# Optimization experiments

Hardware: AMD Instinct MI355X
Metric: run time of the kernel (lower is better)

The kernel has to match this reference:

```python
import jax, jax.numpy as jnp
import numpy as np


def _patch_desc(x, patch_size):
    # x: (n, c, h, w). Replicate-pad by patch_size//2 and gather all
    # patch_size*patch_size shifted views -> (n, c*p*p, h*w) descriptors.
    n, c, h, w = x.shape
    step = patch_size // 2
    y = jnp.pad(x, ((0, 0), (0, 0), (step, step), (step, step)), mode='edge')
    feats = [y[:, :, i:i + h, j:j + w]
             for i in range(patch_size) for j in range(patch_size)]
    d = jnp.stack(feats, axis=2)            # (n, c, p*p, h, w)
    return d.reshape(n, c * patch_size * patch_size, h * w)


def setup_inputs() -> dict:
    key = jax.random.key(0)
    k1, k2 = jax.random.split(key)
    n, c, h, w = 4, 16, 64, 64
    s = jax.random.normal(k1, (n, c, h, w), dtype=jnp.float32)
    t = jax.random.normal(k2, (n, c, h, w), dtype=jnp.float32)
    return {"s": s, "t": t, "patch_size": 3}


def reference(s, t, patch_size):
    n, c, h, w = s.shape
    q = _patch_desc(s, patch_size)          # (n, d, hw) source queries
    p = _patch_desc(t, patch_size)          # (n, d, hw) target points
    # Squared-L2 nearest neighbor per source patch (exact version of FLANN kNN)
    qn = jnp.sum(q * q, axis=1)             # (n, hw)
    pn = jnp.sum(p * p, axis=1)             # (n, hw)
    cross = jnp.einsum('ndi,ndj->nij', q, p)  # (n, hw_q, hw_t)
    d2 = qn[:, :, None] - 2.0 * cross + pn[:, None, :]
    idx = jnp.argmin(d2, axis=2)            # (n, hw) flat target index
    nnd = jnp.min(d2, axis=2)               # (n, hw) squared distance
    idy = idx // w
    idx_x = idx % w
    nnf = jnp.stack([idy.reshape(n, h, w), idx_x.reshape(n, h, w)], axis=1)
    nnd = nnd.reshape(n, 1, h, w)
    return nnf.astype(jnp.int32), nnd
```

## Files before the change

kernel.cpp:

```cpp
#include <hip/hip_runtime.h>


#define N_  4
#define C_  16
#define H_  64
#define W_  64
#define HW_ 4096
#define K_  160
#define SPLITS_M 4
#define KKSTRIDE 528

#define SPLITS_V 4
#define TILES_PER_SPLIT_V 4

typedef _Float16 f16;
typedef _Float16 f16x8 __attribute__((ext_vector_type(8)));
typedef float    f32x4 __attribute__((ext_vector_type(4)));

__device__ __forceinline__ int iclamp(int v, int lo, int hi) {
    return v < lo ? lo : (v > hi ? hi : v);
}

__device__ __forceinline__ void async_ld16(const void* g, void* l) {
    __builtin_amdgcn_global_load_lds(
        (const __attribute__((address_space(1))) unsigned int*)g,
        (__attribute__((address_space(3))) unsigned int*)l, 16, 0, 0);
}

__global__ __launch_bounds__(256)
void build_desc_norms_kernel(const float* __restrict__ s,
                             const float* __restrict__ t,
                             f16* __restrict__ Qh, f16* __restrict__ Ql,
                             f16* __restrict__ Ph, f16* __restrict__ Pl,
                             float* __restrict__ pn,
                             float* __restrict__ qn) {
    const int y0  = blockIdx.x;
    const int n   = blockIdx.y;
    const int src = blockIdx.z;
    const float* img = (src ? s : t) + n * (C_ * HW_);
    f16* Dh = src ? Qh : Ph;
    f16* Dl = src ? Ql : Pl;
    float* nrm = src ? qn : pn;

    __shared__ float imgS[3][C_][W_];
    __shared__ float nS[4][W_];
    const int tid = threadIdx.x;
    #pragma unroll
    for (int k = 0; k < 12; ++k) {
        const int idx = tid + k * 256;
        const int x = idx & 63, c = (idx >> 6) & 15, r = idx >> 10;
        const int gy = iclamp(y0 + r - 1, 0, H_ - 1);
        imgS[r][c][x] = img[c * HW_ + gy * W_ + x];
    }
    __syncthreads();

    const int q = tid >> 6, x = tid & 63;
    const int pix = y0 * W_ + x;
    float nacc = 0.f;
    #pragma unroll
    for (int u = 0; u < 5; ++u) {
        const int kk = q * 5 + u;
        f16x8 hv, lv;
        if (kk < 18) {
            const int d  = kk >> 1;
            const int c0 = (kk & 1) * 8;
            const int dy = (d * 11) >> 5;
            const int dx = d - dy * 3;
            const int xs = iclamp(x + dx - 1, 0, W_ - 1);
            #pragma unroll
            for (int cc = 0; cc < 8; ++cc) {
                const float v = imgS[dy][c0 + cc][xs];
                const f16 h = (f16)v;
                hv[cc] = h;
                lv[cc] = (f16)(v - (float)h);
                nacc += v * v;
            }
        } else {
            #pragma unroll
            for (int cc = 0; cc < 8; ++cc) { hv[cc] = (f16)0.f; lv[cc] = (f16)0.f; }
        }
        const size_t off = ((size_t)(n * 20 + kk) * HW_ + pix) * 8;
        *(f16x8*)&Dh[off] = hv;
        *(f16x8*)&Dl[off] = lv;
    }
    nS[q][x] = nacc;
    __syncthreads();
    if (tid < W_)
        nrm[n * HW_ + pix] = nS[0][tid] + nS[1][tid] + nS[2][tid] + nS[3][tid];
}

__global__ __launch_bounds__(256)
void mfma_nn_kernel(const f16* __restrict__ Qh, const f16* __restrict__ Ql,
                    const f16* __restrict__ Ph, const f16* __restrict__ Pl,
                    const float* __restrict__ pn_g,
                    unsigned long long* __restrict__ partial) {
    const int bid   = blockIdx.x;
    const int split = bid & 3;
    const int n     = (bid >> 2) & 3;
    const int iblk  = bid >> 4;
    const int tid  = threadIdx.x;
    const int wave = tid >> 6, lane = tid & 63;
    const int m = lane & 15, quad = lane >> 4;
    const int irow0 = iblk * 128 + wave * 32;

    __shared__ f16 B0[20 * KKSTRIDE];
    __shared__ f16 B1[20 * KKSTRIDE];
    __shared__ f16 B2[20 * KKSTRIDE];
    __shared__ float pnS[1024];

    f16x8 Ah[2][5], Al[2][5];
    #pragma unroll
    for (int is = 0; is < 2; ++is)
        #pragma unroll
        for (int kc = 0; kc < 5; ++kc) {
            const size_t off = ((size_t)(n * 20 + kc * 4 + quad) * HW_ +
                                irow0 + is * 16 + m) * 8;
            Ah[is][kc] = *(const f16x8*)(Qh + off);
            Al[is][kc] = *(const f16x8*)(Ql + off);
        }

    const int jsplit0 = split * 1024;
    #pragma unroll
    for (int k = 0; k < 4; ++k)
        pnS[tid + k * 256] = pn_g[n * HW_ + jsplit0 + tid + k * 256];

    float    bd[2][4];
    unsigned bj[2][4];
    #pragma unroll
    for (int is = 0; is < 2; ++is)
        #pragma unroll
        for (int rg = 0; rg < 4; ++rg) { bd[is][rg] = 3.0e38f; bj[is][rg] = 0u; }

    const int skk  = wave * 5;
    const int sarr = lane >> 5;
    const int srow = lane & 31;
    const f16* sbase = sarr ? Pl : Ph;

    #define STAGE(BUF, T)                                                     \
        {   _Pragma("unroll")                                                 \
            for (int u = 0; u < 5; ++u) {                                     \
                const int kk = skk + u;                                       \
                const f16* g = sbase + ((size_t)(n * 20 + kk) * HW_ +         \
                                        jsplit0 + (T) * 32 + srow) * 8;       \
                async_ld16(g, (void*)&BUF[kk * KKSTRIDE + lane * 8]);         \
            }                                                                 \
        }

    #define COMPUTE(BUF, T)                                                   \
        {   _Pragma("unroll")                                                 \
            for (int js = 0; js < 2; ++js) {                                  \
                f32x4 Cf[2];                                                  \
                Cf[0] = (f32x4){0.f, 0.f, 0.f, 0.f};                          \
                Cf[1] = (f32x4){0.f, 0.f, 0.f, 0.f};                          \
                _Pragma("unroll")                                             \
                for (int kc = 0; kc < 5; ++kc) {                              \
                    const int kb = (kc * 4 + quad) * KKSTRIDE +               \
                                   (js * 16 + m) * 8;                         \
                    const f16x8 bh = *(const f16x8*)&BUF[kb];                 \
                    const f16x8 bl = *(const f16x8*)&BUF[kb + 256];           \
                    _Pragma("unroll")                                         \
                    for (int is = 0; is < 2; ++is) {                          \
                        Cf[is] = __builtin_amdgcn_mfma_f32_16x16x32_f16(      \
                            Ah[is][kc], bh, Cf[is], 0, 0, 0);                 \
                        Cf[is] = __builtin_amdgcn_mfma_f32_16x16x32_f16(      \
                            Al[is][kc], bh, Cf[is], 0, 0, 0);                 \
                        Cf[is] = __builtin_amdgcn_mfma_f32_16x16x32_f16(      \
                            Ah[is][kc], bl, Cf[is], 0, 0, 0);                 \
                    }                                                         \
                }                                                             \
                const int jloc = (T) * 32 + js * 16 + m;                      \
                const float pnv = pnS[jloc];                                  \
                _Pragma("unroll")                                             \
                for (int is = 0; is < 2; ++is)                                \
                    _Pragma("unroll")                                         \
                    for (int rg = 0; rg < 4; ++rg) {                          \
                        const float d = fmaf(Cf[is][rg], -2.f, pnv);          \
                        if (d < bd[is][rg]) {                                 \
                            bd[is][rg] = d;                                   \
                            bj[is][rg] = (unsigned)jloc;                      \
                        }                                                     \
                    }                                                         \
            }                                                                 \
        }

    STAGE(B0, 0)
    STAGE(B1, 1)
    __syncthreads();

    for (int g = 0; g < 10; ++g) {
        const int t = g * 3;
        asm volatile("s_waitcnt vmcnt(5)" ::: "memory");
        asm volatile("s_barrier" ::: "memory");
        STAGE(B2, t + 2)
        COMPUTE(B0, t)
        asm volatile("s_waitcnt vmcnt(5)" ::: "memory");
        asm volatile("s_barrier" ::: "memory");
        STAGE(B0, t + 3)
        COMPUTE(B1, t + 1)
        asm volatile("s_waitcnt vmcnt(5)" ::: "memory");
        asm volatile("s_barrier" ::: "memory");
        STAGE(B1, t + 4)
        COMPUTE(B2, t + 2)
    }
    asm volatile("s_waitcnt vmcnt(5)" ::: "memory");
    asm volatile("s_barrier" ::: "memory");
    COMPUTE(B0, 30)
    asm volatile("s_waitcnt vmcnt(0)" ::: "memory");
    asm volatile("s_barrier" ::: "memory");
    COMPUTE(B1, 31)
    #undef STAGE
    #undef COMPUTE

    #pragma unroll
    for (int is = 0; is < 2; ++is)
        #pragma unroll
        for (int rg = 0; rg < 4; ++rg) {
            float    d = bd[is][rg];
            unsigned j = (unsigned)jsplit0 + bj[is][rg];
            #pragma unroll
            for (int off = 1; off < 16; off <<= 1) {
                const float    od = __shfl_xor(d, off, 64);
                const unsigned oj = __shfl_xor(j, off, 64);
                const bool take = (od < d) || (od == d && oj < j);
                d = take ? od : d;
                j = take ? oj : j;
            }
            if (m == 0) {
                const int i = irow0 + is * 16 + quad * 4 + rg;
                partial[(size_t)(split * N_ + n) * HW_ + i] =
                    ((unsigned long long)j << 32) |
                    (unsigned long long)__float_as_uint(d);
            }
        }
}

__global__ __launch_bounds__(256)
void finalize_mfma_kernel(const unsigned long long* __restrict__ partial,
                          const float* __restrict__ qn_g,
                          float* __restrict__ out) {
    const int id  = blockIdx.x * 256 + threadIdx.x;
    const int n   = id >> 12;
    const int pix = id & 4095;
    float    bd = 3.0e38f;
    unsigned bj = 0u;
    #pragma unroll
    for (int sp = 0; sp < SPLITS_M; ++sp) {
        const unsigned long long v = partial[(size_t)(sp * N_ + n) * HW_ + pix];
        const float    d = __uint_as_float((unsigned)(v & 0xffffffffull));
        const unsigned j = (unsigned)(v >> 32);
        const bool take = (d < bd) || (d == bd && j < bj);
        bd = take ? d : bd;
        bj = take ? j : bj;
    }
    out[n * 2 * HW_ + pix]            = (float)(bj >> 6);
    out[n * 2 * HW_ + HW_ + pix]      = (float)(bj & 63);
    out[N_ * 2 * HW_ + n * HW_ + pix] = bd + qn_g[n * HW_ + pix];
}

__global__ __launch_bounds__(256)
void prep_norms_kernel(const float* __restrict__ s,
                       const float* __restrict__ t,
                       float* __restrict__ pn,
                       float* __restrict__ qn) {
    const int gid   = blockIdx.x * 256 + threadIdx.x;
    const int which = gid >> 14;
    const int id    = gid & 16383;
    const int n     = id >> 12;
    const int pix   = id & 4095;
    const int y = pix >> 6, x = pix & 63;
    const float* base = (which ? s : t) + n * (C_ * HW_);
    float acc = 0.f;
    for (int c = 0; c < C_; ++c) {
        const float* bc = base + c * HW_;
        #pragma unroll
        for (int dy = 0; dy < 3; ++dy) {
            const float* br = bc + iclamp(y + dy - 1, 0, H_ - 1) * W_;
            #pragma unroll
            for (int dx = 0; dx < 3; ++dx) {
                float v = br[iclamp(x + dx - 1, 0, W_ - 1)];
                acc += v * v;
            }
        }
    }
    (which ? qn : pn)[id] = acc;
}

__global__ __launch_bounds__(256)
void patchmatch_main_kernel(const float* __restrict__ s,
                            const float* __restrict__ t,
                            const float* __restrict__ pn_g,
                            const float* __restrict__ qn_g,
                            unsigned long long* __restrict__ partial) {
    const int yq    = blockIdx.x;
    const int n     = blockIdx.y;
    const int split = blockIdx.z;
    const int tid  = threadIdx.x;
    const int tx   = tid & 15;
    const int ty   = tid >> 4;
    const int i0   = ty * 4;
    const int jrow = tx >> 2;
    const int jx0  = (tx & 3) * 16;

    __shared__ float qS[C_][3][68];
    __shared__ float tS[C_][6][68];
    __shared__ float qnS[W_];

    const float* sb = s + n * (C_ * HW_);
    const float* tb = t + n * (C_ * HW_);

    #pragma unroll
    for (int k = 0; k < 3; ++k) {
        const int id = tid + k * 256;
        const int sg = id & 15;
        const int c  = (id >> 4) & 15;
        const int r  = id >> 8;
        const int gr = iclamp(yq + r - 1, 0, H_ - 1);
        const float4 v = *(const float4*)&sb[c * HW_ + gr * W_ + sg * 4];
        float* dst = &qS[c][r][1 + sg * 4];
        dst[0] = v.x; dst[1] = v.y; dst[2] = v.z; dst[3] = v.w;
    }
    if (tid < 48) {
        const int c  = tid & 15;
        const int r  = tid >> 4;
        const int gr = iclamp(yq + r - 1, 0, H_ - 1);
        qS[c][r][0]  = sb[c * HW_ + gr * W_];
        qS[c][r][65] = sb[c * HW_ + gr * W_ + 63];
    }
    if (tid < W_) qnS[tid] = qn_g[n * HW_ + yq * W_ + tid];

    unsigned long long best[4] = {~0ull, ~0ull, ~0ull, ~0ull};

    for (int ytl = 0; ytl < TILES_PER_SPLIT_V; ++ytl) {
        const int yt = split * TILES_PER_SPLIT_V + ytl;
        __syncthreads();
        #pragma unroll
        for (int k = 0; k < 6; ++k) {
            const int id = tid + k * 256;
            const int sg = id & 15;
            const int c  = (id >> 4) & 15;
            const int r  = id >> 8;
            const int gr = iclamp(4 * yt + r - 1, 0, H_ - 1);
            const float4 v = *(const float4*)&tb[c * HW_ + gr * W_ + sg * 4];
            float* dst = &tS[c][r][1 + sg * 4];
            dst[0] = v.x; dst[1] = v.y; dst[2] = v.z; dst[3] = v.w;
        }
        if (tid < 96) {
            const int c  = tid & 15;
            const int r  = tid >> 4;
            const int gr = iclamp(4 * yt + r - 1, 0, H_ - 1);
            tS[c][r][0]  = tb[c * HW_ + gr * W_];
            tS[c][r][65] = tb[c * HW_ + gr * W_ + 63];
        }
        __syncthreads();

        float acc[4][16];
        #pragma unroll
        for (int a = 0; a < 4; ++a)
            #pragma unroll
            for (int b = 0; b < 16; ++b) acc[a][b] = 0.f;

        for (int c = 0; c < C_; ++c) {
            #pragma unroll
            for (int dy = 0; dy < 3; ++dy) {
                float qv[6], tv[18];
                *(float4*)&qv[0] = *(const float4*)&qS[c][dy][i0];
                *(float2*)&qv[4] = *(const float2*)&qS[c][dy][i0 + 4];
                const float* trow = &tS[c][jrow + dy][jx0];
                *(float4*)&tv[0]  = *(const float4*)&trow[0];
                *(float4*)&tv[4]  = *(const float4*)&trow[4];
                *(float4*)&tv[8]  = *(const float4*)&trow[8];
                *(float4*)&tv[12] = *(const float4*)&trow[12];
                *(float2*)&tv[16] = *(const float2*)&trow[16];
                #pragma unroll
                for (int dx = 0; dx < 3; ++dx)
                    #pragma unroll
                    for (int a = 0; a < 4; ++a)
                        #pragma unroll
                        for (int b = 0; b < 16; ++b)
                            acc[a][b] += qv[a + dx] * tv[b + dx];
            }
        }

        const int jbase = yt * 256 + jrow * W_ + jx0;
        float pnv[16];
        const float* png = &pn_g[n * HW_ + jbase];
        *(float4*)&pnv[0]  = *(const float4*)&png[0];
        *(float4*)&pnv[4]  = *(const float4*)&png[4];
        *(float4*)&pnv[8]  = *(const float4*)&png[8];
        *(float4*)&pnv[12] = *(const float4*)&png[12];
        #pragma unroll
        for (int a = 0; a < 4; ++a) {
            const float qn = qnS[i0 + a];
            #pragma unroll
            for (int b = 0; b < 16; ++b) {
                const float d2 = qn + pnv[b] - 2.f * acc[a][b];
                unsigned long long cand =
                    ((unsigned long long)__float_as_uint(d2) << 32) |
                    (unsigned)(jbase + b);
                best[a] = cand < best[a] ? cand : best[a];
            }
        }
    }

    #pragma unroll
    for (int a = 0; a < 4; ++a) {
        unsigned long long v = best[a];
        #pragma unroll
        for (int mm = 8; mm >= 1; mm >>= 1) {
            unsigned long long o = __shfl_xor(v, mm, 64);
            v = o < v ? o : v;
        }
        best[a] = v;
    }
    if (tx == 0) {
        #pragma unroll
        for (int a = 0; a < 4; ++a)
            partial[((split * N_ + n) * HW_) + yq * W_ + i0 + a] = best[a];
    }
}

__global__ __launch_bounds__(256)
void finalize_kernel(const unsigned long long* __restrict__ partial,
                     float* __restrict__ out) {
    const int id  = blockIdx.x * 256 + threadIdx.x;
    const int n   = id >> 12;
    const int pix = id & 4095;
    unsigned long long best = ~0ull;
    #pragma unroll
    for (int sp = 0; sp < SPLITS_V; ++sp) {
        unsigned long long v = partial[(sp * N_ + n) * HW_ + pix];
        best = v < best ? v : best;
    }
    const unsigned j = (unsigned)(best & 0xffffffffu);
    const float d2 = __uint_as_float((unsigned)(best >> 32));
    out[n * 2 * HW_ + pix]            = (float)(j >> 6);
    out[n * 2 * HW_ + HW_ + pix]      = (float)(j & 63);
    out[N_ * 2 * HW_ + n * HW_ + pix] = d2;
}

__global__ __launch_bounds__(256)
void patchmatch_mono_kernel(const float* __restrict__ s,
                            const float* __restrict__ t,
                            float* __restrict__ out) {
    const int yq  = blockIdx.x;
    const int n   = blockIdx.y;
    const int tid = threadIdx.x;
    const int tx  = tid & 15;
    const int ty  = tid >> 4;
    const int i0  = ty * 4;
    const int jrow = tx >> 3;
    const int jx0  = (tx & 7) * 8;

    __shared__ float qS[C_][3][68];
    __shared__ float tS[C_][4][68];
    __shared__ float pnS[HW_];
    __shared__ float qnS[W_];

    const float* sb = s + n * (C_ * HW_);
    const float* tb = t + n * (C_ * HW_);

    for (int jj = tid; jj < HW_; jj += 256) {
        const int y = jj >> 6, x = jj & 63;
        float acc = 0.f;
        for (int c = 0; c < C_; ++c) {
            const float* tc = tb + c * HW_;
            #pragma unroll
            for (int dy = 0; dy < 3; ++dy) {
                const float* tr = tc + iclamp(y + dy - 1, 0, H_ - 1) * W_;
                #pragma unroll
                for (int dx = 0; dx < 3; ++dx) {
                    float v = tr[iclamp(x + dx - 1, 0, W_ - 1)];
                    acc += v * v;
                }
            }
        }
        pnS[jj] = acc;
    }
    for (int idx = tid; idx < C_ * 3 * 66; idx += 256) {
        const int c   = idx / (3 * 66);
        const int rem = idx - c * (3 * 66);
        const int rr  = rem / 66;
        const int xi  = rem - rr * 66;
        qS[c][rr][xi] = sb[c * HW_ + iclamp(yq + rr - 1, 0, H_ - 1) * W_ +
                           iclamp(xi - 1, 0, W_ - 1)];
    }
    __syncthreads();
    if (tid < W_) {
        float acc = 0.f;
        for (int c = 0; c < C_; ++c)
            #pragma unroll
            for (int dy = 0; dy < 3; ++dy)
                #pragma unroll
                for (int dx = 0; dx < 3; ++dx) {
                    float v = qS[c][dy][tid + dx];
                    acc += v * v;
                }
        qnS[tid] = acc;
    }

    unsigned long long best[4] = {~0ull, ~0ull, ~0ull, ~0ull};
    for (int yt = 0; yt < 32; ++yt) {
        __syncthreads();
        for (int idx = tid; idx < C_ * 4 * 66; idx += 256) {
            const int c   = idx / (4 * 66);
            const int rem = idx - c * (4 * 66);
            const int rr  = rem / 66;
            const int xi  = rem - rr * 66;
            tS[c][rr][xi] = tb[c * HW_ + iclamp(2 * yt + rr - 1, 0, H_ - 1) * W_ +
                               iclamp(xi - 1, 0, W_ - 1)];
        }
        __syncthreads();

        float acc[4][8];
        #pragma unroll
        for (int a = 0; a < 4; ++a)
            #pragma unroll
            for (int b = 0; b < 8; ++b) acc[a][b] = 0.f;

        for (int c = 0; c < C_; ++c) {
            #pragma unroll
            for (int dy = 0; dy < 3; ++dy) {
                float qv[8], tv[12];
                *(float4*)&qv[0] = *(const float4*)&qS[c][dy][i0];
                *(float4*)&qv[4] = *(const float4*)&qS[c][dy][i0 + 4];
                const float* trow = &tS[c][jrow + dy][jx0];
                *(float4*)&tv[0] = *(const float4*)&trow[0];
                *(float4*)&tv[4] = *(const float4*)&trow[4];
                *(float4*)&tv[8] = *(const float4*)&trow[8];
                #pragma unroll
                for (int dx = 0; dx < 3; ++dx)
                    #pragma unroll
                    for (int a = 0; a < 4; ++a)
                        #pragma unroll
                        for (int b = 0; b < 8; ++b)
                            acc[a][b] += qv[a + dx] * tv[b + dx];
            }
        }
        const int rbase = (2 * yt + jrow) * W_ + jx0;
        #pragma unroll
        for (int a = 0; a < 4; ++a) {
            const float qn = qnS[i0 + a];
            #pragma unroll
            for (int b = 0; b < 8; ++b) {
                const int j = rbase + b;
                const float d2 = qn + pnS[j] - 2.f * acc[a][b];
                unsigned long long cand =
                    ((unsigned long long)__float_as_uint(d2) << 32) | (unsigned)j;
                best[a] = cand < best[a] ? cand : best[a];
            }
        }
    }
    #pragma unroll
    for (int a = 0; a < 4; ++a) {
        unsigned long long v = best[a];
        #pragma unroll
        for (int mm = 8; mm >= 1; mm >>= 1) {
            unsigned long long o = __shfl_xor(v, mm, 64);
            v = o < v ? o : v;
        }
        best[a] = v;
    }
    if (tx == 0) {
        #pragma unroll
        for (int a = 0; a < 4; ++a) {
            const int x = i0 + a;
            const unsigned j = (unsigned)(best[a] & 0xffffffffu);
            const float d2 = __uint_as_float((unsigned)(best[a] >> 32));
            const int pix = yq * W_ + x;
            out[n * 2 * HW_ + pix]            = (float)(j >> 6);
            out[n * 2 * HW_ + HW_ + pix]      = (float)(j & 63);
            out[N_ * 2 * HW_ + n * HW_ + pix] = d2;
        }
    }
}

extern "C" void kernel_launch(void* const* d_in, const int* in_sizes, int n_in,
                              void* d_out, int out_size, void* d_ws, size_t ws_size,
                              hipStream_t stream) {
    const float* s = (const float*)d_in[0];
    const float* t = (const float*)d_in[1];
    float* out = (float*)d_out;

    const size_t norm_b  = (size_t)N_ * HW_ * 4;
    const size_t part_b  = (size_t)SPLITS_M * N_ * HW_ * 8;
    const size_t desc_b  = (size_t)N_ * HW_ * K_ * 2;
    const size_t need_m  = 2 * norm_b + part_b + 4 * desc_b;

    if (ws_size >= need_m) {
        char* w = (char*)d_ws;
        float* pn = (float*)w;                       w += norm_b;
        float* qn = (float*)w;                       w += norm_b;
        unsigned long long* partial = (unsigned long long*)w; w += part_b;
        f16* Qh = (f16*)w;  w += desc_b;
        f16* Ql = (f16*)w;  w += desc_b;
        f16* Ph = (f16*)w;  w += desc_b;
        f16* Pl = (f16*)w;

        build_desc_norms_kernel<<<dim3(64, N_, 2), 256, 0, stream>>>(
            s, t, Qh, Ql, Ph, Pl, pn, qn);
        mfma_nn_kernel<<<512, 256, 0, stream>>>(Qh, Ql, Ph, Pl, pn, partial);
        finalize_mfma_kernel<<<64, 256, 0, stream>>>(partial, qn, out);
        return;
    }

    const size_t need_v = 2 * norm_b + (size_t)SPLITS_V * N_ * HW_ * 8;
    if (ws_size >= need_v) {
        float* pn = (float*)d_ws;
        float* qn = pn + N_ * HW_;
        unsigned long long* partial =
            (unsigned long long*)((char*)d_ws + 2 * norm_b);
        prep_norms_kernel<<<128, 256, 0, stream>>>(s, t, pn, qn);
        dim3 grid(H_, N_, SPLITS_V);
        patchmatch_main_kernel<<<grid, 256, 0, stream>>>(s, t, pn, qn, partial);
        finalize_kernel<<<64, 256, 0, stream>>>(partial, out);
        return;
    }

    dim3 grid(H_, N_);
    patchmatch_mono_kernel<<<grid, 256, 0, stream>>>(s, t, out);
}
```

Baseline: 124.8 us.

## Enlarge per-wave query tile to 64 rows, split targets 8 ways, double-buffer

Each wave now holds 64 query rows (4 subtiles) in registers instead of 32, so each staged target tile is reused across twice as many MFMAs. The target range is split 8 ways (512 targets per block) so the grid stays large, and the triple-buffered pipeline with partial vmcnt waits becomes a simpler double buffer with full waits and __syncthreads. It also drops one LDS buffer and adds an occupancy hint of 2 blocks per CU. The larger A-register footprint and accumulators raise register pressure. Full waits before each barrier may expose load latency, and the partial-result buffer and reduction must now handle 8 splits.

```diff
diff --git a/kernel.cpp b/kernel.cpp
--- a/kernel.cpp
+++ b/kernel.cpp
@@ -7,7 +7,7 @@
 #define W_  64
 #define HW_ 4096
 #define K_  160
-#define SPLITS_M 4
+#define SPLITS_M 8
 #define KKSTRIDE 528
 
 #define SPLITS_V 4
@@ -89,28 +89,27 @@
         nrm[n * HW_ + pix] = nS[0][tid] + nS[1][tid] + nS[2][tid] + nS[3][tid];
 }
 
-__global__ __launch_bounds__(256)
+__global__ __launch_bounds__(256, 2)
 void mfma_nn_kernel(const f16* __restrict__ Qh, const f16* __restrict__ Ql,
                     const f16* __restrict__ Ph, const f16* __restrict__ Pl,
                     const float* __restrict__ pn_g,
                     unsigned long long* __restrict__ partial) {
     const int bid   = blockIdx.x;
-    const int split = bid & 3;
-    const int n     = (bid >> 2) & 3;
-    const int iblk  = bid >> 4;
+    const int split = bid & 7;
+    const int n     = (bid >> 3) & 3;
+    const int iblk  = bid >> 5;
     const int tid  = threadIdx.x;
     const int wave = tid >> 6, lane = tid & 63;
     const int m = lane & 15, quad = lane >> 4;
-    const int irow0 = iblk * 128 + wave * 32;
+    const int irow0 = iblk * 256 + wave * 64;
 
     __shared__ f16 B0[20 * KKSTRIDE];
     __shared__ f16 B1[20 * KKSTRIDE];
-    __shared__ f16 B2[20 * KKSTRIDE];
-    __shared__ float pnS[1024];
-
-    f16x8 Ah[2][5], Al[2][5];
-    #pragma unroll
-    for (int is = 0; is < 2; ++is)
+    __shared__ float pnS[512];
+
+    f16x8 Ah[4][5], Al[4][5];
+    #pragma unroll
+    for (int is = 0; is < 4; ++is)
         #pragma unroll
         for (int kc = 0; kc < 5; ++kc) {
             const size_t off = ((size_t)(n * 20 + kc * 4 + quad) * HW_ +
@@ -119,15 +118,14 @@
             Al[is][kc] = *(const f16x8*)(Ql + off);
         }
 
-    const int jsplit0 = split * 1024;
-    #pragma unroll
-    for (int k = 0; k < 4; ++k)
-        pnS[tid + k * 256] = pn_g[n * HW_ + jsplit0 + tid + k * 256];
-
-    float    bd[2][4];
-    unsigned bj[2][4];
-    #pragma unroll
-    for (int is = 0; is < 2; ++is)
+    const int jsplit0 = split * 512;
+    pnS[tid]       = pn_g[n * HW_ + jsplit0 + tid];
+    pnS[tid + 256] = pn_g[n * HW_ + jsplit0 + tid + 256];
+
+    float    bd[4][4];
+    unsigned bj[4][4];
+    #pragma unroll
+    for (int is = 0; is < 4; ++is)
         #pragma unroll
         for (int rg = 0; rg < 4; ++rg) { bd[is][rg] = 3.0e38f; bj[is][rg] = 0u; }
 
@@ -149,9 +147,10 @@
     #define COMPUTE(BUF, T)                                                   \
         {   _Pragma("unroll")                                                 \
             for (int js = 0; js < 2; ++js) {                                  \
-                f32x4 Cf[2];                                                  \
-                Cf[0] = (f32x4){0.f, 0.f, 0.f, 0.f};                          \
-                Cf[1] = (f32x4){0.f, 0.f, 0.f, 0.f};                          \
+                f32x4 Cf[4];                                                  \
+                _Pragma("unroll")                                             \
+                for (int is = 0; is < 4; ++is)                                \
+                    Cf[is] = (f32x4){0.f, 0.f, 0.f, 0.f};                     \
                 _Pragma("unroll")                                             \
                 for (int kc = 0; kc < 5; ++kc) {                              \
                     const int kb = (kc * 4 + quad) * KKSTRIDE +               \
@@ -159,7 +158,7 @@
                     const f16x8 bh = *(const f16x8*)&BUF[kb];                 \
                     const f16x8 bl = *(const f16x8*)&BUF[kb + 256];           \
                     _Pragma("unroll")                                         \
-                    for (int is = 0; is < 2; ++is) {                          \
+                    for (int is = 0; is < 4; ++is) {                          \
                         Cf[is] = __builtin_amdgcn_mfma_f32_16x16x32_f16(      \
                             Ah[is][kc], bh, Cf[is], 0, 0, 0);                 \
                         Cf[is] = __builtin_amdgcn_mfma_f32_16x16x32_f16(      \
@@ -171,11 +170,11 @@
                 const int jloc = (T) * 32 + js * 16 + m;                      \
                 const float pnv = pnS[jloc];                                  \
                 _Pragma("unroll")                                             \
-                for (int is = 0; is < 2; ++is)                                \
+                for (int is = 0; is < 4; ++is)                                \
                     _Pragma("unroll")                                         \
                     for (int rg = 0; rg < 4; ++rg) {                          \
                         const float d = fmaf(Cf[is][rg], -2.f, pnv);          \
-                        if (d < bd[is][rg]) {                                 \
+                        if (d < bd[is][rg]) {       \
                             bd[is][rg] = d;                                   \
                             bj[is][rg] = (unsigned)jloc;                      \
                         }                                                     \
@@ -184,35 +183,24 @@
         }
 
     STAGE(B0, 0)
-    STAGE(B1, 1)
+    asm volatile("s_waitcnt vmcnt(0)" ::: "memory");
     __syncthreads();
 
-    for (int g = 0; g < 10; ++g) {
-        const int t = g * 3;
-        asm volatile("s_waitcnt vmcnt(5)" ::: "memory");
-        asm volatile("s_barrier" ::: "memory");
-        STAGE(B2, t + 2)
-        COMPUTE(B0, t)
-        asm volatile("s_waitcnt vmcnt(5)" ::: "memory");
-        asm volatile("s_barrier" ::: "memory");
-        STAGE(B0, t + 3)
-        COMPUTE(B1, t + 1)
-        asm volatile("s_waitcnt vmcnt(5)" ::: "memory");
-        asm volatile("s_barrier" ::: "memory");
-        STAGE(B1, t + 4)
-        COMPUTE(B2, t + 2)
-    }
-    asm volatile("s_waitcnt vmcnt(5)" ::: "memory");
-    asm volatile("s_barrier" ::: "memory");
-    COMPUTE(B0, 30)
-    asm volatile("s_waitcnt vmcnt(0)" ::: "memory");
-    asm volatile("s_barrier" ::: "memory");
-    COMPUTE(B1, 31)
+    for (int jt = 0; jt < 16; jt += 2) {
+        if (jt + 1 < 16) STAGE(B1, jt + 1)
+        COMPUTE(B0, jt)
+        asm volatile("s_waitcnt vmcnt(0)" ::: "memory");
+        __syncthreads();
+        if (jt + 2 < 16) STAGE(B0, jt + 2)
+        COMPUTE(B1, jt + 1)
+        asm volatile("s_waitcnt vmcnt(0)" ::: "memory");
+        __syncthreads();
+    }
     #undef STAGE
     #undef COMPUTE
 
     #pragma unroll
-    for (int is = 0; is < 2; ++is)
+    for (int is = 0; is < 4; ++is)
         #pragma unroll
         for (int rg = 0; rg < 4; ++rg) {
             float    d = bd[is][rg];
```

Result: no change. 127.2 us (+1.9%).

## Switch to double-buffered LDS tiles with phase-staggered order and register prefetch

Applied to the files above, without the earlier changes.

Replaces the triple-buffered LDS pipeline, which used partial vmcnt waits, with a double buffer that does a full vmcnt(0) wait and a __syncthreads per tile. It also starts each block at a different tile offset depending on block-id bit 8, presumably to spread L2 and HBM accesses. Inside COMPUTE, the B-fragment reads from LDS are software-pipelined one step ahead of the MFMAs, and accumulators are kept for both column halves. The argmin update now uses an explicit tie-break on the lower index so results stay deterministic when the tile order rotates. The trade is less LDS use, which may allow higher occupancy, against a shallower prefetch depth and stronger synchronisation.

```diff
diff --git a/kernel.cpp b/kernel.cpp
--- a/kernel.cpp
+++ b/kernel.cpp
@@ -98,6 +98,7 @@
     const int split = bid & 3;
     const int n     = (bid >> 2) & 3;
     const int iblk  = bid >> 4;
+    const int phase = (bid >> 8) & 1;
     const int tid  = threadIdx.x;
     const int wave = tid >> 6, lane = tid & 63;
     const int m = lane & 15, quad = lane >> 4;
@@ -105,7 +106,6 @@
 
     __shared__ f16 B0[20 * KKSTRIDE];
     __shared__ f16 B1[20 * KKSTRIDE];
-    __shared__ f16 B2[20 * KKSTRIDE];
     __shared__ float pnS[1024];
 
     f16x8 Ah[2][5], Al[2][5];
@@ -129,12 +129,13 @@
     #pragma unroll
     for (int is = 0; is < 2; ++is)
         #pragma unroll
-        for (int rg = 0; rg < 4; ++rg) { bd[is][rg] = 3.0e38f; bj[is][rg] = 0u; }
+        for (int rg = 0; rg < 4; ++rg) { bd[is][rg] = 3.0e38f; bj[is][rg] = ~0u; }
 
     const int skk  = wave * 5;
-    const int sarr = lane >> 5;
     const int srow = lane & 31;
-    const f16* sbase = sarr ? Pl : Ph;
+    const f16* sbase = (lane >> 5) ? Pl : Ph;
+
+    #define TILE(T) (((T) + (phase << 4)) & 31)
 
     #define STAGE(BUF, T)                                                     \
         {   _Pragma("unroll")                                                 \
@@ -147,69 +148,70 @@
         }
 
     #define COMPUTE(BUF, T)                                                   \
-        {   _Pragma("unroll")                                                 \
+        {   f32x4 Cf[2][2];                                                   \
+            Cf[0][0] = (f32x4){0.f, 0.f, 0.f, 0.f};                           \
+            Cf[0][1] = (f32x4){0.f, 0.f, 0.f, 0.f};                           \
+            Cf[1][0] = (f32x4){0.f, 0.f, 0.f, 0.f};                           \
+            Cf[1][1] = (f32x4){0.f, 0.f, 0.f, 0.f};                           \
+            f16x8 cbh, cbl, nbh, nbl;                                         \
+            cbh = *(const f16x8*)&BUF[quad * KKSTRIDE + m * 8];               \
+            cbl = *(const f16x8*)&BUF[quad * KKSTRIDE + m * 8 + 256];         \
+            _Pragma("unroll")                                                 \
+            for (int g = 0; g < 10; ++g) {                                    \
+                const int js = g / 5, kc = g - js * 5;                        \
+                if (g < 9) {                                                  \
+                    const int gn = g + 1;                                     \
+                    const int jsn = gn / 5, kcn = gn - jsn * 5;               \
+                    const int kbn = (kcn * 4 + quad) * KKSTRIDE +             \
+                                    (jsn * 16 + m) * 8;                      \
+                    nbh = *(const f16x8*)&BUF[kbn];                           \
+                    nbl = *(const f16x8*)&BUF[kbn + 256];                     \
+                }                                                             \
+                _Pragma("unroll")                                             \
+                for (int is = 0; is < 2; ++is) {                              \
+                    Cf[is][js] = __builtin_amdgcn_mfma_f32_16x16x32_f16(      \
+                        Ah[is][kc], cbh, Cf[is][js], 0, 0, 0);                \
+                    Cf[is][js] = __builtin_amdgcn_mfma_f32_16x16x32_f16(      \
+                        Al[is][kc], cbh, Cf[is][js], 0, 0, 0);                \
+                    Cf[is][js] = __builtin_amdgcn_mfma_f32_16x16x32_f16(      \
+                        Ah[is][kc], cbl, Cf[is][js], 0, 0, 0);                \
+                }                                                             \
+                cbh = nbh; cbl = nbl;                                         \
+            }                                                                 \
+            _Pragma("unroll")                                                 \
             for (int js = 0; js < 2; ++js) {                                  \
-                f32x4 Cf[2];                                                  \
-                Cf[0] = (f32x4){0.f, 0.f, 0.f, 0.f};                          \
-                Cf[1] = (f32x4){0.f, 0.f, 0.f, 0.f};                          \
-                _Pragma("unroll")                                             \
-                for (int kc = 0; kc < 5; ++kc) {                              \
-                    const int kb = (kc * 4 + quad) * KKSTRIDE +               \
-                                   (js * 16 + m) * 8;                         \
-                    const f16x8 bh = *(const f16x8*)&BUF[kb];                 \
-                    const f16x8 bl = *(const f16x8*)&BUF[kb + 256];           \
-                    _Pragma("unroll")                                         \
-                    for (int is = 0; is < 2; ++is) {                          \
-                        Cf[is] = __builtin_amdgcn_mfma_f32_16x16x32_f16(      \
-                            Ah[is][kc], bh, Cf[is], 0, 0, 0);                 \
-                        Cf[is] = __builtin_amdgcn_mfma_f32_16x16x32_f16(      \
-                            Al[is][kc], bh, Cf[is], 0, 0, 0);                 \
-                        Cf[is] = __builtin_amdgcn_mfma_f32_16x16x32_f16(      \
-                            Ah[is][kc], bl, Cf[is], 0, 0, 0);                 \
-                    }                                                         \
-                }                                                             \
-                const int jloc = (T) * 32 + js * 16 + m;                      \
+                const unsigned jloc = (unsigned)((T) * 32 + js * 16 + m);     \
                 const float pnv = pnS[jloc];                                  \
                 _Pragma("unroll")                                             \
                 for (int is = 0; is < 2; ++is)                                \
                     _Pragma("unroll")                                         \
                     for (int rg = 0; rg < 4; ++rg) {                          \
-                        const float d = fmaf(Cf[is][rg], -2.f, pnv);          \
-                        if (d < bd[is][rg]) {                                 \
-                            bd[is][rg] = d;                                   \
-                            bj[is][rg] = (unsigned)jloc;                      \
-                        }                                                     \
+                        const float d = fmaf(Cf[is][js][rg], -2.f, pnv);      \
+                        const bool take = (d < bd[is][rg]) ||                 \
+                            (d == bd[is][rg] && jloc < bj[is][rg]);           \
+                        bd[is][rg] = take ? d : bd[is][rg];                   \
+                        bj[is][rg] = take ? jloc : bj[is][rg];                \
                     }                                                         \
             }                                                                 \
         }
 
-    STAGE(B0, 0)
-    STAGE(B1, 1)
+    STAGE(B0, TILE(0))
+    asm volatile("s_waitcnt vmcnt(0)" ::: "memory");
     __syncthreads();
 
-    for (int g = 0; g < 10; ++g) {
-        const int t = g * 3;
-        asm volatile("s_waitcnt vmcnt(5)" ::: "memory");
-        asm volatile("s_barrier" ::: "memory");
-        STAGE(B2, t + 2)
-        COMPUTE(B0, t)
-        asm volatile("s_waitcnt vmcnt(5)" ::: "memory");
-        asm volatile("s_barrier" ::: "memory");
-        STAGE(B0, t + 3)
-        COMPUTE(B1, t + 1)
-        asm volatile("s_waitcnt vmcnt(5)" ::: "memory");
-        asm volatile("s_barrier" ::: "memory");
-        STAGE(B1, t + 4)
-        COMPUTE(B2, t + 2)
-    }
-    asm volatile("s_waitcnt vmcnt(5)" ::: "memory");
-    asm volatile("s_barrier" ::: "memory");
-    COMPUTE(B0, 30)
-    asm volatile("s_waitcnt vmcnt(0)" ::: "memory");
-    asm volatile("s_barrier" ::: "memory");
-    COMPUTE(B1, 31)
+    for (int tl = 0; tl < 32; tl += 2) {
+        if (tl + 1 < 32) STAGE(B1, TILE(tl + 1))
+        COMPUTE(B0, TILE(tl))
+        asm volatile("s_waitcnt vmcnt(0)" ::: "memory");
+        __syncthreads();
+        if (tl + 2 < 32) STAGE(B0, TILE(tl + 2))
+        COMPUTE(B1, TILE(tl + 1))
+        asm volatile("s_waitcnt vmcnt(0)" ::: "memory");
+        __syncthreads();
+    }
     #undef STAGE
     #undef COMPUTE
+    #undef TILE
 
     #pragma unroll
     for (int is = 0; is < 2; ++is)
```

Measured after the change: 130.0 us. +4.2%, slower.

## Fuse descriptor, MFMA search and finalize into one cooperative kernel

Applied to the files above, without the earlier changes.

Merges the three launches (descriptor build, MFMA nearest-neighbour search, finalize) into a single cooperative kernel with grid-wide syncs, so two kernel launches and their gaps disappear. To fit the shared-memory budget for occupancy, the MFMA stage drops from triple to double buffering with full vmcnt(0) waits and __syncthreads, and the LDS row stride shrinks. The fallback vector path is removed. The grid syncs and weaker prefetch pipelining may cost more than the launch overhead saved, and host-side attribute and occupancy queries now run on every call.

```diff
diff --git a/kernel.cpp b/kernel.cpp
--- a/kernel.cpp
+++ b/kernel.cpp
@@ -1,4 +1,7 @@
 #include <hip/hip_runtime.h>
+#include <hip/hip_cooperative_groups.h>
+
+namespace cg = cooperative_groups;
 
 
 #define N_  4
@@ -8,7 +11,7 @@
 #define HW_ 4096
 #define K_  160
 #define SPLITS_M 4
-#define KKSTRIDE 528
+#define KKSTRIDE 520
 
 #define SPLITS_V 4
 #define TILES_PER_SPLIT_V 4
@@ -27,24 +30,20 @@
         (__attribute__((address_space(3))) unsigned int*)l, 16, 0, 0);
 }
 
-__global__ __launch_bounds__(256)
-void build_desc_norms_kernel(const float* __restrict__ s,
-                             const float* __restrict__ t,
-                             f16* __restrict__ Qh, f16* __restrict__ Ql,
-                             f16* __restrict__ Ph, f16* __restrict__ Pl,
-                             float* __restrict__ pn,
-                             float* __restrict__ qn) {
-    const int y0  = blockIdx.x;
-    const int n   = blockIdx.y;
-    const int src = blockIdx.z;
+
+__device__ __forceinline__
+void desc_phase(char* smem, int y0, int n, int src, int tid,
+                const float* __restrict__ s, const float* __restrict__ t,
+                f16* __restrict__ Qh, f16* __restrict__ Ql,
+                f16* __restrict__ Ph, f16* __restrict__ Pl,
+                float* __restrict__ pn, float* __restrict__ qn) {
+    float (*imgS)[C_][W_] = (float(*)[C_][W_])smem;
+    float (*nS)[W_]       = (float(*)[W_])(smem + 12288);
     const float* img = (src ? s : t) + n * (C_ * HW_);
     f16* Dh = src ? Qh : Ph;
     f16* Dl = src ? Ql : Pl;
     float* nrm = src ? qn : pn;
 
-    __shared__ float imgS[3][C_][W_];
-    __shared__ float nS[4][W_];
-    const int tid = threadIdx.x;
     #pragma unroll
     for (int k = 0; k < 12; ++k) {
         const int idx = tid + k * 256;
@@ -89,24 +88,19 @@
         nrm[n * HW_ + pix] = nS[0][tid] + nS[1][tid] + nS[2][tid] + nS[3][tid];
 }
 
-__global__ __launch_bounds__(256)
-void mfma_nn_kernel(const f16* __restrict__ Qh, const f16* __restrict__ Ql,
-                    const f16* __restrict__ Ph, const f16* __restrict__ Pl,
-                    const float* __restrict__ pn_g,
-                    unsigned long long* __restrict__ partial) {
-    const int bid   = blockIdx.x;
-    const int split = bid & 3;
-    const int n     = (bid >> 2) & 3;
-    const int iblk  = bid >> 4;
-    const int tid  = threadIdx.x;
+__device__ __forceinline__
+void mfma_phase(char* smem, int split, int n, int iblk, int tid,
+                const f16* __restrict__ Qh, const f16* __restrict__ Ql,
+                const f16* __restrict__ Ph, const f16* __restrict__ Pl,
+                const float* __restrict__ pn_g,
+                unsigned long long* __restrict__ partial) {
+    f16*   B0  = (f16*)smem;
+    f16*   B1  = (f16*)(smem + 20 * KKSTRIDE * 2);
+    float* pnS = (float*)(smem + 40 * KKSTRIDE * 2);
+
     const int wave = tid >> 6, lane = tid & 63;
     const int m = lane & 15, quad = lane >> 4;
     const int irow0 = iblk * 128 + wave * 32;
-
-    __shared__ f16 B0[20 * KKSTRIDE];
-    __shared__ f16 B1[20 * KKSTRIDE];
-    __shared__ f16 B2[20 * KKSTRIDE];
-    __shared__ float pnS[1024];
 
     f16x8 Ah[2][5], Al[2][5];
     #pragma unroll
@@ -132,9 +126,8 @@
         for (int rg = 0; rg < 4; ++rg) { bd[is][rg] = 3.0e38f; bj[is][rg] = 0u; }
 
     const int skk  = wave * 5;
-    const int sarr = lane >> 5;
     const int srow = lane & 31;
-    const f16* sbase = sarr ? Pl : Ph;
+    const f16* sbase = (lane >> 5) ? Pl : Ph;
 
     #define STAGE(BUF, T)                                                     \
         {   _Pragma("unroll")                                                 \
@@ -175,7 +168,7 @@
                     _Pragma("unroll")                                         \
                     for (int rg = 0; rg < 4; ++rg) {                          \
                         const float d = fmaf(Cf[is][rg], -2.f, pnv);          \
-                        if (d < bd[is][rg]) {                                 \
+                        if (d < bd[is][rg]) {       \
                             bd[is][rg] = d;                                   \
                             bj[is][rg] = (unsigned)jloc;                      \
                         }                                                     \
@@ -184,30 +177,19 @@
         }
 
     STAGE(B0, 0)
-    STAGE(B1, 1)
+    asm volatile("s_waitcnt vmcnt(0)" ::: "memory");
     __syncthreads();
 
-    for (int g = 0; g < 10; ++g) {
-        const int t = g * 3;
-        asm volatile("s_waitcnt vmcnt(5)" ::: "memory");
-        asm volatile("s_barrier" ::: "memory");
-        STAGE(B2, t + 2)
-        COMPUTE(B0, t)
-        asm volatile("s_waitcnt vmcnt(5)" ::: "memory");
-        asm volatile("s_barrier" ::: "memory");
-        STAGE(B0, t + 3)
-        COMPUTE(B1, t + 1)
-        asm volatile("s_waitcnt vmcnt(5)" ::: "memory");
-        asm volatile("s_barrier" ::: "memory");
-        STAGE(B1, t + 4)
-        COMPUTE(B2, t + 2)
-    }
-    asm volatile("s_waitcnt vmcnt(5)" ::: "memory");
-    asm volatile("s_barrier" ::: "memory");
-    COMPUTE(B0, 30)
-    asm volatile("s_waitcnt vmcnt(0)" ::: "memory");
-    asm volatile("s_barrier" ::: "memory");
-    COMPUTE(B1, 31)
+    for (int jt = 0; jt < 32; jt += 2) {
+        if (jt + 1 < 32) STAGE(B1, jt + 1)
+        COMPUTE(B0, jt)
+        asm volatile("s_waitcnt vmcnt(0)" ::: "memory");
+        __syncthreads();
+        if (jt + 2 < 32) STAGE(B0, jt + 2)
+        COMPUTE(B1, jt + 1)
+        asm volatile("s_waitcnt vmcnt(0)" ::: "memory");
+        __syncthreads();
+    }
     #undef STAGE
     #undef COMPUTE
 
@@ -234,11 +216,9 @@
         }
 }
 
-__global__ __launch_bounds__(256)
-void finalize_mfma_kernel(const unsigned long long* __restrict__ partial,
-                          const float* __restrict__ qn_g,
-                          float* __restrict__ out) {
-    const int id  = blockIdx.x * 256 + threadIdx.x;
+__device__ __forceinline__
+void finalize_phase(int id, const unsigned long long* __restrict__ partial,
+                    const float* __restrict__ qn_g, float* __restrict__ out) {
     const int n   = id >> 12;
     const int pix = id & 4095;
     float    bd = 3.0e38f;
@@ -258,184 +238,58 @@
 }
 
 __global__ __launch_bounds__(256)
-void prep_norms_kernel(const float* __restrict__ s,
-                       const float* __restrict__ t,
-                       float* __restrict__ pn,
-                       float* __restrict__ qn) {
-    const int gid   = blockIdx.x * 256 + threadIdx.x;
-    const int which = gid >> 14;
-    const int id    = gid & 16383;
-    const int n     = id >> 12;
-    const int pix   = id & 4095;
-    const int y = pix >> 6, x = pix & 63;
-    const float* base = (which ? s : t) + n * (C_ * HW_);
-    float acc = 0.f;
-    for (int c = 0; c < C_; ++c) {
-        const float* bc = base + c * HW_;
-        #pragma unroll
-        for (int dy = 0; dy < 3; ++dy) {
-            const float* br = bc + iclamp(y + dy - 1, 0, H_ - 1) * W_;
-            #pragma unroll
-            for (int dx = 0; dx < 3; ++dx) {
-                float v = br[iclamp(x + dx - 1, 0, W_ - 1)];
-                acc += v * v;
-            }
-        }
-    }
-    (which ? qn : pn)[id] = acc;
+void fused_nn_kernel(const float* __restrict__ s, const float* __restrict__ t,
+                     f16* __restrict__ Qh, f16* __restrict__ Ql,
+                     f16* __restrict__ Ph, f16* __restrict__ Pl,
+                     float* __restrict__ pn, float* __restrict__ qn,
+                     unsigned long long* __restrict__ partial,
+                     float* __restrict__ out) {
+    __shared__ __align__(16) char smem[45696];
+    const int bid = blockIdx.x;
+    const int tid = threadIdx.x;
+    cg::grid_group grid = cg::this_grid();
+
+    desc_phase(smem, bid & 63, (bid >> 6) & 3, bid >> 8, tid,
+               s, t, Qh, Ql, Ph, Pl, pn, qn);
+    __threadfence();
+    grid.sync();
+
+    mfma_phase(smem, bid & 3, (bid >> 2) & 3, bid >> 4, tid,
+               Qh, Ql, Ph, Pl, pn, partial);
+    __threadfence();
+    grid.sync();
+
+    if (bid < 64) finalize_phase(bid * 256 + tid, partial, qn, out);
 }
 
 __global__ __launch_bounds__(256)
-void patchmatch_main_kernel(const float* __restrict__ s,
-                            const float* __restrict__ t,
-                            const float* __restrict__ pn_g,
-                            const float* __restrict__ qn_g,
-                            unsigned long long* __restrict__ partial) {
-    const int yq    = blockIdx.x;
-    const int n     = blockIdx.y;
-    const int split = blockIdx.z;
-    const int tid  = threadIdx.x;
-    const int tx   = tid & 15;
-    const int ty   = tid >> 4;
-    const int i0   = ty * 4;
-    const int jrow = tx >> 2;
-    const int jx0  = (tx & 3) * 16;
-
-    __shared__ float qS[C_][3][68];
-    __shared__ float tS[C_][6][68];
-    __shared__ float qnS[W_];
-
-    const float* sb = s + n * (C_ * HW_);
-    const float* tb = t + n * (C_ * HW_);
-
-    #pragma unroll
-    for (int k = 0; k < 3; ++k) {
-        const int id = tid + k * 256;
-        const int sg = id & 15;
-        const int c  = (id >> 4) & 15;
-        const int r  = id >> 8;
-        const int gr = iclamp(yq + r - 1, 0, H_ - 1);
-        const float4 v = *(const float4*)&sb[c * HW_ + gr * W_ + sg * 4];
-        float* dst = &qS[c][r][1 + sg * 4];
-        dst[0] = v.x; dst[1] = v.y; dst[2] = v.z; dst[3] = v.w;
-    }
-    if (tid < 48) {
-        const int c  = tid & 15;
-        const int r  = tid >> 4;
-        const int gr = iclamp(yq + r - 1, 0, H_ - 1);
-        qS[c][r][0]  = sb[c * HW_ + gr * W_];
-        qS[c][r][65] = sb[c * HW_ + gr * W_ + 63];
-    }
-    if (tid < W_) qnS[tid] = qn_g[n * HW_ + yq * W_ + tid];
-
-    unsigned long long best[4] = {~0ull, ~0ull, ~0ull, ~0ull};
-
-    for (int ytl = 0; ytl < TILES_PER_SPLIT_V; ++ytl) {
-        const int yt = split * TILES_PER_SPLIT_V + ytl;
-        __syncthreads();
-        #pragma unroll
-        for (int k = 0; k < 6; ++k) {
-            const int id = tid + k * 256;
-            const int sg = id & 15;
-            const int c  = (id >> 4) & 15;
-            const int r  = id >> 8;
-            const int gr = iclamp(4 * yt + r - 1, 0, H_ - 1);
-            const float4 v = *(const float4*)&tb[c * HW_ + gr * W_ + sg * 4];
-            float* dst = &tS[c][r][1 + sg * 4];
-            dst[0] = v.x; dst[1] = v.y; dst[2] = v.z; dst[3] = v.w;
-        }
-        if (tid < 96) {
-            const int c  = tid & 15;
-            const int r  = tid >> 4;
-            const int gr = iclamp(4 * yt + r - 1, 0, H_ - 1);
-            tS[c][r][0]  = tb[c * HW_ + gr * W_];
-            tS[c][r][65] = tb[c * HW_ + gr * W_ + 63];
-        }
-        __syncthreads();
-
-        float acc[4][16];
-        #pragma unroll
-        for (int a = 0; a < 4; ++a)
-            #pragma unroll
-            for (int b = 0; b < 16; ++b) acc[a][b] = 0.f;
-
-        for (int c = 0; c < C_; ++c) {
-            #pragma unroll
-            for (int dy = 0; dy < 3; ++dy) {
-                float qv[6], tv[18];
-                *(float4*)&qv[0] = *(const float4*)&qS[c][dy][i0];
-                *(float2*)&qv[4] = *(const float2*)&qS[c][dy][i0 + 4];
-                const float* trow = &tS[c][jrow + dy][jx0];
-                *(float4*)&tv[0]  = *(const float4*)&trow[0];
-                *(float4*)&tv[4]  = *(const float4*)&trow[4];
-                *(float4*)&tv[8]  = *(const float4*)&trow[8];
-                *(float4*)&tv[12] = *(const float4*)&trow[12];
-                *(float2*)&tv[16] = *(const float2*)&trow[16];
-                #pragma unroll
-                for (int dx = 0; dx < 3; ++dx)
-                    #pragma unroll
-                    for (int a = 0; a < 4; ++a)
-                        #pragma unroll
-                        for (int b = 0; b < 16; ++b)
-                            acc[a][b] += qv[a + dx] * tv[b + dx];
-            }
-        }
-
-        const int jbase = yt * 256 + jrow * W_ + jx0;
-        float pnv[16];
-        const float* png = &pn_g[n * HW_ + jbase];
-        *(float4*)&pnv[0]  = *(const float4*)&png[0];
-        *(float4*)&pnv[4]  = *(const float4*)&png[4];
-        *(float4*)&pnv[8]  = *(const float4*)&png[8];
-        *(float4*)&pnv[12] = *(const float4*)&png[12];
-        #pragma unroll
-        for (int a = 0; a < 4; ++a) {
-            const float qn = qnS[i0 + a];
-            #pragma unroll
-            for (int b = 0; b < 16; ++b) {
-                const float d2 = qn + pnv[b] - 2.f * acc[a][b];
-                unsigned long long cand =
-                    ((unsigned long long)__float_as_uint(d2) << 32) |
-                    (unsigned)(jbase + b);
-                best[a] = cand < best[a] ? cand : best[a];
-            }
-        }
-    }
-
-    #pragma unroll
-    for (int a = 0; a < 4; ++a) {
-        unsigned long long v = best[a];
-        #pragma unroll
-        for (int mm = 8; mm >= 1; mm >>= 1) {
-            unsigned long long o = __shfl_xor(v, mm, 64);
-            v = o < v ? o : v;
-        }
-        best[a] = v;
-    }
-    if (tx == 0) {
-        #pragma unroll
-        for (int a = 0; a < 4; ++a)
-            partial[((split * N_ + n) * HW_) + yq * W_ + i0 + a] = best[a];
-    }
+void build_desc_norms_kernel(const float* __restrict__ s,
+                             const float* __restrict__ t,
+                             f16* __restrict__ Qh, f16* __restrict__ Ql,
+                             f16* __restrict__ Ph, f16* __restrict__ Pl,
+                             float* __restrict__ pn,
+                             float* __restrict__ qn) {
+    __shared__ __align__(16) char smem[13312];
+    desc_phase(smem, blockIdx.x, blockIdx.y, blockIdx.z, threadIdx.x,
+               s, t, Qh, Ql, Ph, Pl, pn, qn);
 }
 
 __global__ __launch_bounds__(256)
-void finalize_kernel(const unsigned long long* __restrict__ partial,
-                     float* __restrict__ out) {
-    const int id  = blockIdx.x * 256 + threadIdx.x;
-    const int n   = id >> 12;
-    const int pix = id & 4095;
-    unsigned long long best = ~0ull;
-    #pragma unroll
-    for (int sp = 0; sp < SPLITS_V; ++sp) {
-        unsigned long long v = partial[(sp * N_ + n) * HW_ + pix];
-        best = v < best ? v : best;
-    }
-    const unsigned j = (unsigned)(best & 0xffffffffu);
-    const float d2 = __uint_as_float((unsigned)(best >> 32));
-    out[n * 2 * HW_ + pix]            = (float)(j >> 6);
-    out[n * 2 * HW_ + HW_ + pix]      = (float)(j & 63);
-    out[N_ * 2 * HW_ + n * HW_ + pix] = d2;
+void mfma_nn_kernel(const f16* __restrict__ Qh, const f16* __restrict__ Ql,
+                    const f16* __restrict__ Ph, const f16* __restrict__ Pl,
+                    const float* __restrict__ pn_g,
+                    unsigned long long* __restrict__ partial) {
+    __shared__ __align__(16) char smem[45696];
+    const int bid = blockIdx.x;
+    mfma_phase(smem, bid & 3, (bid >> 2) & 3, bid >> 4, threadIdx.x,
+               Qh, Ql, Ph, Pl, pn_g, partial);
+}
+
+__global__ __launch_bounds__(256)
+void finalize_mfma_kernel(const unsigned long long* __restrict__ partial,
+                          const float* __restrict__ qn_g,
+                          float* __restrict__ out) {
+    finalize_phase(blockIdx.x * 256 + threadIdx.x, partial, qn_g, out);
 }
 
 __global__ __launch_bounds__(256)
@@ -596,6 +450,28 @@
         f16* Ph = (f16*)w;  w += desc_b;
         f16* Pl = (f16*)w;
 
+        int dev = 0;
+        (void)hipGetDevice(&dev);
+        int coop = 0;
+        (void)hipDeviceGetAttribute(&coop, hipDeviceAttributeCooperativeLaunch,
+                                    dev);
+        int nCU = 0;
+        (void)hipDeviceGetAttribute(&nCU, hipDeviceAttributeMultiprocessorCount,
+                                    dev);
+        int maxBlk = 0;
+        (void)hipOccupancyMaxActiveBlocksPerMultiprocessor(
+            &maxBlk, (const void*)fused_nn_kernel, 256, 0);
+
+        if (coop && (long long)maxBlk * nCU >= 512) {
+            void* args[] = { (void*)&s, (void*)&t, (void*)&Qh, (void*)&Ql,
+                             (void*)&Ph, (void*)&Pl, (void*)&pn, (void*)&qn,
+                             (void*)&partial, (void*)&out };
+            hipError_t err = hipLaunchCooperativeKernel(
+                (const void*)fused_nn_kernel, dim3(512), dim3(256), args, 0,
+                stream);
+            if (err == hipSuccess) return;
+        }
+
         build_desc_norms_kernel<<<dim3(64, N_, 2), 256, 0, stream>>>(
             s, t, Qh, Ql, Ph, Pl, pn, qn);
         mfma_nn_kernel<<<512, 256, 0, stream>>>(Qh, Ql, Ph, Pl, pn, partial);
@@ -603,19 +479,6 @@
         return;
     }
 
-    const size_t need_v = 2 * norm_b + (size_t)SPLITS_V * N_ * HW_ * 8;
-    if (ws_size >= need_v) {
-        float* pn = (float*)d_ws;
-        float* qn = pn + N_ * HW_;
-        unsigned long long* partial =
-            (unsigned long long*)((char*)d_ws + 2 * norm_b);
-        prep_norms_kernel<<<128, 256, 0, stream>>>(s, t, pn, qn);
-        dim3 grid(H_, N_, SPLITS_V);
-        patchmatch_main_kernel<<<grid, 256, 0, stream>>>(s, t, pn, qn, partial);
-        finalize_kernel<<<64, 256, 0, stream>>>(partial, out);
-        return;
-    }
-
     dim3 grid(H_, N_);
     patchmatch_mono_kernel<<<grid, 256, 0, stream>>>(s, t, out);
 }
```

New measurement: 126.0 us. About the same (+1.0%).
